# Optimization experiments

Measured on AMD Instinct MI355X. Metric: run time of the kernel, lower is better.

## Reference

```python
import jax, jax.numpy as jnp
import numpy as np

HEADS = 8
SCALE_BASE = 512
EPS = 1e-5


def xpos(x, downscale=False):
    # x: (B, h, S, hd) ; XPOS rotary embedding with exponential scale
    hd = x.shape[-1]
    S = x.shape[-2]
    half = hd // 2
    base_scale = (jnp.arange(0, hd, 2, dtype=jnp.float32) + 0.4 * hd) / (1.4 * hd)  # (half,)
    pos = jnp.arange(S, dtype=jnp.float32)
    scale = base_scale[None, :] ** (pos[:, None] / SCALE_BASE)  # (S, half)
    inv_freq = 1.0 / (10000.0 ** (jnp.arange(half, dtype=jnp.float32) / half))
    sinu = pos[:, None] * inv_freq[None, :]  # (S, half)
    sin, cos = jnp.sin(sinu), jnp.cos(sinu)
    if downscale:
        scale = 1.0 / scale
    # duplicate_interleave: (S, half) -> (S, hd)
    sin_s = jnp.repeat(sin * scale, 2, axis=-1)
    cos_s = jnp.repeat(cos * scale, 2, axis=-1)
    x1 = x[..., ::2]
    x2 = x[..., 1::2]
    rot = jnp.stack((-x2, x1), axis=-1).reshape(x.shape)  # rotate_every_two
    return x * cos_s + rot * sin_s


def decay_mask(S):
    # (heads, S, S): gamma^(n-m) for n>=m else 0
    gammas = 1.0 - jnp.exp(jnp.linspace(np.log(1 / 32), np.log(1 / 512), HEADS)).astype(jnp.float32)
    n = jnp.arange(S, dtype=jnp.float32)
    diff = n[:, None] - n[None, :]
    lg = jnp.log(gammas)[:, None, None]
    return jnp.where(diff >= 0, jnp.exp(jnp.maximum(diff, 0.0) * lg), 0.0)


def layer_norm(x, w, b):
    mu = x.mean(-1, keepdims=True)
    var = x.var(-1, keepdims=True)
    return (x - mu) / jnp.sqrt(var + EPS) * w + b


def multiscale_retention(Xq, Xkv, Wq, Wk, Wv, Wg, Wo, gn_w, gn_b):
    # Xq: (B,S,d) query source; Xkv: (B,S,d) key/value source (== Xq for self)
    B, S, _ = Xq.shape
    Q = jnp.einsum('bsd,hde->bhse', Xq, Wq)
    K = jnp.einsum('btd,hde->bhte', Xkv, Wk)
    V = jnp.einsum('btd,hdv->bhtv', Xkv, Wv)
    Q = xpos(Q)
    K = xpos(K, downscale=True)
    D = decay_mask(S)  # (h,S,S)
    scores = jnp.einsum('bhse,bhte->bhst', Q, K) * D[None]
    Y = jnp.einsum('bhst,bhtv->bhsv', scores, V)  # (B,h,S,hv)
    h, hv = Y.shape[1], Y.shape[3]
    # GroupNorm(heads, v_dim) over each head's channels per token
    mu = Y.mean(-1, keepdims=True)
    var = Y.var(-1, keepdims=True)
    Yn = (Y - mu) / jnp.sqrt(var + EPS)
    Yn = Yn.transpose(0, 2, 1, 3).reshape(B, S, h * hv) * gn_w + gn_b
    gate = jax.nn.sigmoid(Xq @ Wg) * (Xq @ Wg)  # swish gate
    return (gate * Yn) @ Wo


def setup_inputs() -> dict:
    key = jax.random.key(0)
    ks = jax.random.split(key, 32)
    d, f, h, hd, hv, vd = 1024, 4096, 8, 128, 256, 2048
    B, S = 2, 2048
    inp = {
        'X': jax.random.normal(ks[0], (B, S, d), jnp.float32),
        'mem': jax.random.normal(ks[1], (B, S, d), jnp.float32),
        'ln1_w': jax.random.uniform(ks[2], (d,), jnp.float32, 0.5, 1.5),
        'ln1_b': jax.random.normal(ks[3], (d,), jnp.float32) * 0.1,
        'ln2_w': jax.random.uniform(ks[4], (d,), jnp.float32, 0.5, 1.5),
        'ln2_b': jax.random.normal(ks[5], (d,), jnp.float32) * 0.1,
        'Wq': jax.random.normal(ks[6], (h, d, hd), jnp.float32) / d,
        'Wk': jax.random.normal(ks[7], (h, d, hd), jnp.float32) / d,
        'Wv': jax.random.normal(ks[8], (h, d, hv), jnp.float32) / d,
        'Wg': jax.random.normal(ks[9], (d, vd), jnp.float32) / d,
        'Wo': jax.random.normal(ks[10], (vd, d), jnp.float32) / d,
        'gn_w': jax.random.uniform(ks[11], (vd,), jnp.float32, 0.5, 1.5),
        'gn_b': jax.random.normal(ks[12], (vd,), jnp.float32) * 0.1,
        'cWq': jax.random.normal(ks[13], (h, d, hd), jnp.float32) / d,
        'cWk': jax.random.normal(ks[14], (h, d, hd), jnp.float32) / d,
        'cWv': jax.random.normal(ks[15], (h, d, hv), jnp.float32) / d,
        'cWg': jax.random.normal(ks[16], (d, vd), jnp.float32) / d,
        'cWo': jax.random.normal(ks[17], (vd, d), jnp.float32) / d,
        'cgn_w': jax.random.uniform(ks[18], (vd,), jnp.float32, 0.5, 1.5),
        'cgn_b': jax.random.normal(ks[19], (vd,), jnp.float32) * 0.1,
        'W1': jax.random.normal(ks[20], (d, f), jnp.float32) * (1.0 / np.sqrt(d)),
        'b1': jax.random.normal(ks[21], (f,), jnp.float32) * 0.02,
        'W2': jax.random.normal(ks[22], (f, d), jnp.float32) * (1.0 / np.sqrt(f)),
        'b2': jax.random.normal(ks[23], (d,), jnp.float32) * 0.02,
    }
    return inp


def reference(X, mem, ln1_w, ln1_b, ln2_w, ln2_b, Wq, Wk, Wv, Wg, Wo, gn_w, gn_b,
              cWq, cWk, cWv, cWg, cWo, cgn_w, cgn_b, W1, b1, W2, b2):
    # self retention block
    X = multiscale_retention(layer_norm(X, ln1_w, ln1_b), None, Wq, Wk, Wv, Wg, Wo, gn_w, gn_b) + X if False else multiscale_retention(layer_norm(X, ln1_w, ln1_b), layer_norm(X, ln1_w, ln1_b), Wq, Wk, Wv, Wg, Wo, gn_w, gn_b) + X
    # cross retention block (note: original reuses layer_norms_2 for both this and the FFN)
    h2 = layer_norm(X, ln2_w, ln2_b)
    X = multiscale_retention(h2, mem, cWq, cWk, cWv, cWg, cWo, cgn_w, cgn_b) + X
    # FFN block (GELU exact, per torch nn.GELU default)
    h3 = layer_norm(X, ln2_w, ln2_b)
    X = (jax.nn.gelu(h3 @ W1 + b1, approximate=False) @ W2 + b2) + X
    return X
```

## Files before the change

### kernel.cpp

```cpp
#include <hip/hip_runtime.h>
#include <math.h>

#define RTOT 4096
#define SEQQ 2048

typedef unsigned int uint32;
typedef __attribute__((ext_vector_type(4))) float f32x4;
typedef __attribute__((ext_vector_type(8))) short bf16x8;

__device__ __forceinline__ unsigned short f2bf(float f) {
  unsigned int u = __float_as_uint(f);
  u = (u + 0x7FFFu + ((u >> 16) & 1u)) >> 16;
  return (unsigned short)u;
}
__device__ __forceinline__ float bf2f(unsigned short h) {
  return __uint_as_float(((unsigned int)h) << 16);
}
__device__ __forceinline__ void gld16(const void* g, void* l) {
  __builtin_amdgcn_global_load_lds(
      (const __attribute__((address_space(1))) uint32*)g,
      (__attribute__((address_space(3))) uint32*)l, 16, 0, 0);
}
__device__ __forceinline__ void bar() {
  asm volatile("" ::: "memory");
  __builtin_amdgcn_s_barrier();
  asm volatile("" ::: "memory");
}
#define VMCNT(n) asm volatile("s_waitcnt vmcnt(" #n ")" ::: "memory")

__device__ __forceinline__ void tr_tile(
    const float* __restrict__ in, unsigned short* __restrict__ out,
    int R, int C, int perm, int bx, int by, int z) {
  __shared__ float t[32][33];
  in  += (size_t)z * R * C;
  out += (size_t)z * C * R;
  int r0 = bx * 32, c0 = by * 32;
  int tx = threadIdx.x & 31, ty = threadIdx.x >> 5;
  #pragma unroll
  for (int i = 0; i < 4; ++i) {
    int r = ty + i * 8;
    t[r][tx] = in[(size_t)(r0 + r) * C + c0 + tx];
  }
  __syncthreads();
  #pragma unroll
  for (int i = 0; i < 4; ++i) {
    int cc = c0 + ty + i * 8;
    if (perm) cc = 64 * (cc >> 6) + ((cc & 1) << 5) + ((cc & 63) >> 1);
    out[(size_t)cc * R + r0 + tx] = f2bf(t[tx][ty + i * 8]);
  }
}

__device__ __forceinline__ void tab_body(float* __restrict__ tab, int blk) {
  int i = blk * 256 + threadIdx.x;
  int pos = i >> 6, j = i & 63;
  float bs = (2.f * (float)j + 51.2f) * (1.f / 179.2f);
  float e = (float)pos * (1.f / 512.f);
  float sc = exp2f(e * log2f(bs));
  float invf = exp2f(-(float)j * (13.287712379549449f / 64.f));
  float su, cu;
  sincosf((float)pos * invf, &su, &cu);
  tab[i]            = cu * sc;
  tab[131072 + i]   = su * sc;
  float si = 1.f / sc;
  tab[262144 + i]   = cu * si;
  tab[393216 + i]   = su * si;
}

__global__ __launch_bounds__(256) void prep1(
    const float* Wq, const float* Wk, const float* Wg, const float* Wv,
    const float* Wo, unsigned short* WqkgT, unsigned short* WvT,
    unsigned short* WoT, float* tab) {
  int idx = blockIdx.x;
  if (idx < 1024)      { tr_tile(Wq, WqkgT,               1024, 128, 1, idx & 31, (idx >> 5) & 3, idx >> 7); }
  else if (idx < 2048) { int i = idx - 1024; tr_tile(Wk, WqkgT + 1024 * 1024, 1024, 128, 1, i & 31, (i >> 5) & 3, i >> 7); }
  else if (idx < 4096) { int i = idx - 2048; tr_tile(Wg, WqkgT + 2048 * 1024, 1024, 2048, 0, i & 31, i >> 5, 0); }
  else if (idx < 6144) { int i = idx - 4096; tr_tile(Wv, WvT, 1024, 256, 0, i & 31, (i >> 5) & 7, i >> 8); }
  else if (idx < 8192) { int i = idx - 6144; tr_tile(Wo, WoT, 2048, 1024, 0, i & 63, i >> 6, 0); }
  else                 { tab_body(tab, idx - 8192); }
}

__global__ __launch_bounds__(256) void prep2(
    const float* cWq, const float* cWg, const float* cWk, const float* cWv,
    const float* cWo, unsigned short* cQGT, unsigned short* cWkT,
    unsigned short* cWvT, unsigned short* cWoT) {
  int idx = blockIdx.x;
  if (idx < 1024)      { tr_tile(cWq, cQGT,               1024, 128, 1, idx & 31, (idx >> 5) & 3, idx >> 7); }
  else if (idx < 3072) { int i = idx - 1024; tr_tile(cWg, cQGT + 1024 * 1024, 1024, 2048, 0, i & 31, i >> 5, 0); }
  else if (idx < 4096) { int i = idx - 3072; tr_tile(cWk, cWkT, 1024, 128, 1, i & 31, (i >> 5) & 3, i >> 7); }
  else if (idx < 6144) { int i = idx - 4096; tr_tile(cWv, cWvT, 1024, 256, 0, i & 31, (i >> 5) & 7, i >> 8); }
  else                 { int i = idx - 6144; tr_tile(cWo, cWoT, 2048, 1024, 0, i & 63, i >> 6, 0); }
}

__global__ __launch_bounds__(256) void prep3(
    const float* W1, const float* W2, unsigned short* W1T, unsigned short* W2T) {
  int idx = blockIdx.x;
  if (idx < 4096) { tr_tile(W1, W1T, 1024, 4096, 0, idx & 31, idx >> 5, 0); }
  else            { int i = idx - 4096; tr_tile(W2, W2T, 4096, 1024, 0, i & 127, i >> 7, 0); }
}

__global__ __launch_bounds__(256) void cvt_bf16(
    const float* __restrict__ in, unsigned short* __restrict__ out, int n8) {
  int i = blockIdx.x * 256 + threadIdx.x;
  if (i >= n8) return;
  const float4* p = (const float4*)(in + (size_t)i * 8);
  float4 a = p[0], b = p[1];
  bf16x8 v;
  v[0] = (short)f2bf(a.x); v[1] = (short)f2bf(a.y); v[2] = (short)f2bf(a.z); v[3] = (short)f2bf(a.w);
  v[4] = (short)f2bf(b.x); v[5] = (short)f2bf(b.y); v[6] = (short)f2bf(b.z); v[7] = (short)f2bf(b.w);
  *(bf16x8*)(out + (size_t)i * 8) = v;
}

__global__ __launch_bounds__(256) void ln_bf16(const float* __restrict__ x,
    const float* __restrict__ w, const float* __restrict__ b,
    unsigned short* __restrict__ out) {
  int row = blockIdx.x, tid = threadIdx.x;
  const float* xr = x + (size_t)row * 1024;
  float4 v = *(const float4*)(xr + tid * 4);
  float s  = v.x + v.y + v.z + v.w;
  float ss = v.x*v.x + v.y*v.y + v.z*v.z + v.w*v.w;
  #pragma unroll
  for (int o = 32; o > 0; o >>= 1) { s += __shfl_down(s, o); ss += __shfl_down(ss, o); }
  __shared__ float red[2][4];
  int wid = tid >> 6;
  if ((tid & 63) == 0) { red[0][wid] = s; red[1][wid] = ss; }
  __syncthreads();
  float st  = red[0][0] + red[0][1] + red[0][2] + red[0][3];
  float sst = red[1][0] + red[1][1] + red[1][2] + red[1][3];
  float mu   = st * (1.f / 1024.f);
  float var  = sst * (1.f / 1024.f) - mu * mu;
  float rstd = rsqrtf(var + 1e-5f);
  float4 wv = *(const float4*)(w + tid * 4);
  float4 bv = *(const float4*)(b + tid * 4);
  unsigned short o0 = f2bf((v.x - mu) * rstd * wv.x + bv.x);
  unsigned short o1 = f2bf((v.y - mu) * rstd * wv.y + bv.y);
  unsigned short o2 = f2bf((v.z - mu) * rstd * wv.z + bv.z);
  unsigned short o3 = f2bf((v.w - mu) * rstd * wv.w + bv.w);
  ushort4 o4 = make_ushort4(o0, o1, o2, o3);
  *(ushort4*)(out + (size_t)row * 1024 + tid * 4) = o4;
}

enum { EPI_F32_RES = 0, EPI_BF16 = 1, EPI_XPOS = 2, EPI_GELU = 4, EPI_BRES = 5,
       EPI_QKG = 6, EPI_QG = 7 };

struct EpiP {
  void* C; int ldc;
  const float* bias; const float* resid;
  const float* tab;
  unsigned short* oQ; unsigned short* oK; unsigned short* oG;
};

template<int EPI>
__device__ __forceinline__ void epi_store(size_t m, int n, int N0, float v, const EpiP& P) {
  if constexpr (EPI == EPI_BF16) {
    ((unsigned short*)P.C)[m * P.ldc + n] = f2bf(v);
  } else if constexpr (EPI == EPI_GELU) {
    v += P.bias[n];
    v = 0.5f * v * (1.f + erff(v * 0.70710678f));
    ((unsigned short*)P.C)[m * P.ldc + n] = f2bf(v);
  } else if constexpr (EPI == EPI_BRES) {
    v += P.bias[n] + P.resid[m * P.ldc + n];
    ((float*)P.C)[m * P.ldc + n] = v;
  } else {
    v += P.resid[m * P.ldc + n];
    ((float*)P.C)[m * P.ldc + n] = v;
  }
}

template<int EPI>
__global__ __launch_bounds__(256) void gemm_mfma(
    const unsigned short* __restrict__ A, int lda,
    const unsigned short* __restrict__ Bt, int ldb, int K, int nbx, EpiP P) {
  __shared__ __align__(16) unsigned short As[2][2][128 * 32];
  __shared__ __align__(16) unsigned short Bs[2][2][128 * 32];
  const int tid = threadIdx.x, w = tid >> 6, lane = tid & 63;
  int q8 = (int)gridDim.x >> 3;
  int sbid = ((int)blockIdx.x & 7) * q8 + ((int)blockIdx.x >> 3);
  int by = sbid / nbx, bx = sbid - by * nbx;
  const int M0 = by * 128, N0 = bx * 128;
  const int fr = lane & 15, fs = lane >> 4;
  const int srow = lane >> 2, sp = lane & 3;

  f32x4 zf = {0.f, 0.f, 0.f, 0.f};
  f32x4 acc[4][4];
  #pragma unroll
  for (int i = 0; i < 4; ++i)
    #pragma unroll
    for (int j = 0; j < 4; ++j) acc[i][j] = zf;

  auto STAGE = [&](int buf, int k0) {
    #pragma unroll
    for (int kk = 0; kk < 2; ++kk)
      #pragma unroll
      for (int c = 0; c < 4; ++c) {
        int ch = w * 4 + c;
        int cc = ch & 7;
        int row = cc * 16 + srow;
        int so = sp ^ ((row >> 1) & 3);
        if (ch < 8) gld16(A  + (size_t)(M0 + row) * lda + k0 + kk * 32 + so * 8, &As[buf][kk][cc * 512]);
        else        gld16(Bt + (size_t)(N0 + row) * ldb + k0 + kk * 32 + so * 8, &Bs[buf][kk][cc * 512]);
      }
  };

  const int NT = K >> 6;
  STAGE(0, 0);
  int cur = 0;
  for (int t = 0; t < NT; ++t) {
    if (t + 1 < NT) { STAGE(cur ^ 1, (t + 1) * 64); VMCNT(8); }
    else            { VMCNT(0); }
    bar();
    #pragma unroll
    for (int kk = 0; kk < 2; ++kk) {
      bf16x8 af[4], bfr[4];
      #pragma unroll
      for (int mi = 0; mi < 4; ++mi) {
        int row = (w >> 1) * 64 + mi * 16 + fr;
        af[mi] = *(const bf16x8*)(&As[cur][kk][row * 32 + (fs ^ ((row >> 1) & 3)) * 8]);
      }
      #pragma unroll
      for (int ni = 0; ni < 4; ++ni) {
        int row = (w & 1) * 64 + ni * 16 + fr;
        bfr[ni] = *(const bf16x8*)(&Bs[cur][kk][row * 32 + (fs ^ ((row >> 1) & 3)) * 8]);
      }
      #pragma unroll
      for (int mi = 0; mi < 4; ++mi)
        #pragma unroll
        for (int ni = 0; ni < 4; ++ni)
          acc[mi][ni] = __builtin_amdgcn_mfma_f32_16x16x32_bf16(af[mi], bfr[ni], acc[mi][ni], 0, 0, 0);
    }
    bar();
    cur ^= 1;
  }

  #pragma unroll
  for (int mi = 0; mi < 4; ++mi)
    #pragma unroll
    for (int r = 0; r < 4; ++r) {
      size_t m = M0 + (w >> 1) * 64 + mi * 16 + fs * 4 + r;
      #pragma unroll
      for (int ni = 0; ni < 4; ++ni) {
        int n = N0 + (w & 1) * 64 + ni * 16 + fr;
        epi_store<EPI>(m, n, N0, acc[mi][ni][r], P);
      }
    }
}

template<int EPI>
__global__ __launch_bounds__(256) void gemm_bn64(
    const unsigned short* __restrict__ A, int lda,
    const unsigned short* __restrict__ Bt, int ldb, int K, int nbx, EpiP P) {
  __shared__ __align__(16) unsigned short As[2][2][128 * 32];
  __shared__ __align__(16) unsigned short Bs[2][2][64 * 32];
  const int tid = threadIdx.x, w = tid >> 6, lane = tid & 63;
  int q8 = (int)gridDim.x >> 3;
  int sbid = ((int)blockIdx.x & 7) * q8 + ((int)blockIdx.x >> 3);
  int by = sbid / nbx, bx = sbid - by * nbx;
  const int M0 = by * 128, N0 = bx * 64;
  const int fr = lane & 15, fs = lane >> 4;
  const int srow = lane >> 2, sp = lane & 3;

  f32x4 zf = {0.f, 0.f, 0.f, 0.f};
  f32x4 acc[2][4];
  #pragma unroll
  for (int i = 0; i < 2; ++i)
    #pragma unroll
    for (int j = 0; j < 4; ++j) acc[i][j] = zf;

  auto STAGE = [&](int buf, int k0) {
    #pragma unroll
    for (int kk = 0; kk < 2; ++kk)
      #pragma unroll
      for (int c = 0; c < 3; ++c) {
        int ch = w * 3 + c;
        if (ch < 8) {
          int row = ch * 16 + srow;
          int so = sp ^ ((row >> 1) & 3);
          gld16(A + (size_t)(M0 + row) * lda + k0 + kk * 32 + so * 8, &As[buf][kk][ch * 512]);
        } else {
          int bch = ch - 8;
          int row = bch * 16 + srow;
          int so = sp ^ ((row >> 1) & 3);
          gld16(Bt + (size_t)(N0 + row) * ldb + k0 + kk * 32 + so * 8, &Bs[buf][kk][bch * 512]);
        }
      }
  };

  const int NT = K >> 6;
  STAGE(0, 0);
  int cur = 0;
  for (int t = 0; t < NT; ++t) {
    if (t + 1 < NT) { STAGE(cur ^ 1, (t + 1) * 64); VMCNT(6); }
    else            { VMCNT(0); }
    bar();
    #pragma unroll
    for (int kk = 0; kk < 2; ++kk) {
      bf16x8 af[2], bfr[4];
      #pragma unroll
      for (int mi = 0; mi < 2; ++mi) {
        int row = w * 32 + mi * 16 + fr;
        af[mi] = *(const bf16x8*)(&As[cur][kk][row * 32 + (fs ^ ((row >> 1) & 3)) * 8]);
      }
      #pragma unroll
      for (int ni = 0; ni < 4; ++ni) {
        int row = ni * 16 + fr;
        bfr[ni] = *(const bf16x8*)(&Bs[cur][kk][row * 32 + (fs ^ ((row >> 1) & 3)) * 8]);
      }
      #pragma unroll
      for (int mi = 0; mi < 2; ++mi)
        #pragma unroll
        for (int ni = 0; ni < 4; ++ni)
          acc[mi][ni] = __builtin_amdgcn_mfma_f32_16x16x32_bf16(af[mi], bfr[ni], acc[mi][ni], 0, 0, 0);
    }
    bar();
    cur ^= 1;
  }

  if constexpr (EPI == EPI_XPOS) {
    int gsel = (N0 >> 6) & 1;
    #pragma unroll
    for (int mi = 0; mi < 2; ++mi)
      #pragma unroll
      for (int r = 0; r < 4; ++r) {
        size_t m = M0 + w * 32 + mi * 16 + fs * 4 + r;
        int pos = (int)(m & (SEQQ - 1));
        #pragma unroll
        for (int ni = 0; ni < 2; ++ni) {
          int j = gsel * 32 + ni * 16 + fr;
          float cs = P.tab[pos * 64 + j], sn = P.tab[131072 + pos * 64 + j];
          float ve = acc[mi][ni][r], vo = acc[mi][ni + 2][r];
          unsigned short* dst = (unsigned short*)P.C;
          dst[m * P.ldc + N0 + ni * 16 + fr]       = f2bf(ve * cs - vo * sn);
          dst[m * P.ldc + N0 + (ni + 2) * 16 + fr] = f2bf(vo * cs + ve * sn);
        }
      }
  } else {
    #pragma unroll
    for (int mi = 0; mi < 2; ++mi)
      #pragma unroll
      for (int r = 0; r < 4; ++r) {
        size_t m = M0 + w * 32 + mi * 16 + fs * 4 + r;
        #pragma unroll
        for (int ni = 0; ni < 4; ++ni) {
          int n = N0 + ni * 16 + fr;
          epi_store<EPI>(m, n, N0, acc[mi][ni][r], P);
        }
      }
  }
}

template<int EPI>
__global__ __launch_bounds__(512, 2) void gemm256(
    const unsigned short* __restrict__ A,
    const unsigned short* __restrict__ Bt,
    int nbx, EpiP P) {
  __shared__ __align__(16) unsigned short lds[4][2][8192];
  const int tid = threadIdx.x, w = tid >> 6, lane = tid & 63;
  int cpx = (int)gridDim.x >> 3;
  int sbid = ((int)blockIdx.x & 7) * cpx + ((int)blockIdx.x >> 3);
  int by = sbid / nbx, bx = sbid - by * nbx;
  const int M0 = by * 256, N0 = bx * 256;
  const int wm = w >> 2, wn = w & 3;
  const int fr = lane & 15, fs = lane >> 4;
  const int srow = lane >> 2;
  const int sslot = (lane & 3) ^ ((lane >> 3) & 3);
  const int rsw = (fr >> 1) & 3;

  f32x4 acc[8][4];
  #pragma unroll
  for (int i = 0; i < 8; ++i)
    #pragma unroll
    for (int j = 0; j < 4; ++j) acc[i][j] = {0.f, 0.f, 0.f, 0.f};

  auto STAGE = [&](int t, int buf) {
    int k0 = t * 32;
    #pragma unroll
    for (int j = 0; j < 4; ++j) {
      int c = w * 4 + j;
      if (c < 16)
        gld16(A  + (size_t)(M0 + c * 16 + srow) * 1024 + k0 + sslot * 8,
              &lds[buf][0][c * 512]);
      else
        gld16(Bt + (size_t)(N0 + (c - 16) * 16 + srow) * 1024 + k0 + sslot * 8,
              &lds[buf][1][(c - 16) * 512]);
    }
  };
  auto COMPUTE = [&](int t) {
    const unsigned short* la = &lds[t & 3][0][wm * 128 * 32];
    const unsigned short* lb = &lds[t & 3][1][wn * 64 * 32];
    bf16x8 a[8], b[4];
    #pragma unroll
    for (int ni = 0; ni < 4; ++ni)
      b[ni] = *(const bf16x8*)(lb + (ni * 16 + fr) * 32 + ((fs ^ rsw) * 8));
    #pragma unroll
    for (int mi = 0; mi < 8; ++mi)
      a[mi] = *(const bf16x8*)(la + (mi * 16 + fr) * 32 + ((fs ^ rsw) * 8));
    #pragma unroll
    for (int mi = 0; mi < 8; ++mi)
      #pragma unroll
      for (int ni = 0; ni < 4; ++ni)
        acc[mi][ni] = __builtin_amdgcn_mfma_f32_16x16x32_bf16(a[mi], b[ni], acc[mi][ni], 0, 0, 0);
  };

  STAGE(0, 0); STAGE(1, 1); STAGE(2, 2);
  for (int t = 0; t < 29; ++t) {
    STAGE(t + 3, (t + 3) & 3);
    VMCNT(12);
    bar();
    COMPUTE(t);
    bar();
  }
  VMCNT(8);  bar(); COMPUTE(29); bar();
  VMCNT(4);  bar(); COMPUTE(30); bar();
  VMCNT(0);  bar(); COMPUTE(31);

  if constexpr (EPI == EPI_GELU) {
    #pragma unroll
    for (int mi = 0; mi < 8; ++mi)
      #pragma unroll
      for (int r = 0; r < 4; ++r) {
        size_t m = M0 + wm * 128 + mi * 16 + fs * 4 + r;
        #pragma unroll
        for (int ni = 0; ni < 4; ++ni) {
          int n = N0 + wn * 64 + ni * 16 + fr;
          float v = acc[mi][ni][r] + P.bias[n];
          v = 0.5f * v * (1.f + erff(v * 0.70710678f));
          ((unsigned short*)P.C)[m * P.ldc + n] = f2bf(v);
        }
      }
  } else {
    const int nb = N0 + wn * 64;
    const bool isQ = nb < 1024;
    const bool isK = (EPI == EPI_QKG) && !isQ && (nb < 2048);
    if (isQ || isK) {
      const float* tc = isK ? P.tab + 262144 : P.tab;
      const float* ts = tc + 131072;
      unsigned short* dst = isK ? P.oK : P.oQ;
      const int nloc = isK ? nb - 1024 : nb;
      const int gsel = (nloc >> 6) & 1;
      #pragma unroll
      for (int mi = 0; mi < 8; ++mi)
        #pragma unroll
        for (int r = 0; r < 4; ++r) {
          size_t m = M0 + wm * 128 + mi * 16 + fs * 4 + r;
          int pos = (int)(m & (SEQQ - 1));
          #pragma unroll
          for (int ni = 0; ni < 2; ++ni) {
            int j = gsel * 32 + ni * 16 + fr;
            float cs = tc[pos * 64 + j], sn = ts[pos * 64 + j];
            float ve = acc[mi][ni][r], vo = acc[mi][ni + 2][r];
            dst[m * 1024 + nloc + ni * 16 + fr]       = f2bf(ve * cs - vo * sn);
            dst[m * 1024 + nloc + (ni + 2) * 16 + fr] = f2bf(vo * cs + ve * sn);
          }
        }
    } else {
      const int nloc = nb - ((EPI == EPI_QKG) ? 2048 : 1024);
      #pragma unroll
      for (int mi = 0; mi < 8; ++mi)
        #pragma unroll
        for (int r = 0; r < 4; ++r) {
          size_t m = M0 + wm * 128 + mi * 16 + fs * 4 + r;
          #pragma unroll
          for (int ni = 0; ni < 4; ++ni) {
            float v = acc[mi][ni][r];
            P.oG[m * 2048 + nloc + ni * 16 + fr] = f2bf(v / (1.f + expf(-v)));
          }
        }
    }
  }
}

__global__ __launch_bounds__(256) void retention_part(
    const unsigned short* __restrict__ Qx, const unsigned short* __restrict__ Kx,
    const unsigned short* __restrict__ VT,
    unsigned short* __restrict__ Y0, unsigned short* __restrict__ Y1) {
  __shared__ __align__(16) unsigned short Ks[2][32 * 128];
  __shared__ __align__(16) unsigned short Vs[2][256 * 32];
  const int tid = threadIdx.x, w = tid >> 6, lane = tid & 63;
  int bid = blockIdx.x;
  int th = bid >> 9;
  int rr = bid & 511;
  int qt, h, b;
  if (rr < 256) { qt = 31 - (rr >> 3); h = rr & 7; b = 0; }
  else          { int k = rr - 256; qt = k >> 3; h = k & 7; b = 1; }
  const int q0 = qt * 64;
  const int fr = lane & 15, fs = lane >> 4;

  float gamma = 1.f - expf(-3.4657359028f - 0.3960841032f * (float)h);
  float l2g = log2f(gamma);
  const int qglob = q0 + w * 16 + fr;

  size_t qrow = (size_t)b * SEQQ + qglob;
  bf16x8 qf[4];
  #pragma unroll
  for (int ks = 0; ks < 4; ++ks)
    qf[ks] = *(const bf16x8*)(Qx + qrow * 1024 + h * 128 + ks * 32 + fs * 8);

  float gtl8[8];
  #pragma unroll
  for (int i = 0; i < 8; ++i) {
    int toff = (i >> 2) * 16 + fs * 4 + (i & 3);
    gtl8[i] = exp2f(-(float)toff * l2g);
  }

  f32x4 zf = {0.f, 0.f, 0.f, 0.f};
  f32x4 yacc[16];
  #pragma unroll
  for (int i = 0; i < 16; ++i) yacc[i] = zf;

  int cutoff = (int)(16.f / (-l2g));
  int t_start = q0 - cutoff;
  if (t_start < 0) t_start = 0;
  t_start &= ~31;
  size_t kbase = (size_t)b * SEQQ;

  auto STAGE = [&](int buf, int t0) {
    #pragma unroll
    for (int c = 0; c < 2; ++c) {
      int ch = w * 2 + c;
      int row = ch * 4 + (lane >> 4);
      int so = (lane & 15) ^ (row & 15);
      gld16(Kx + (kbase + t0 + row) * 1024 + h * 128 + so * 8, &Ks[buf][ch * 512]);
    }
    #pragma unroll
    for (int c = 0; c < 4; ++c) {
      int ch = w * 4 + c;
      int vrow = ch * 16 + (lane >> 2);
      int so = (lane & 3) ^ ((vrow >> 1) & 3);
      gld16(VT + (size_t)(h * 256 + vrow) * RTOT + kbase + t0 + so * 8, &Vs[buf][ch * 512]);
    }
  };

  const int nt_total = (q0 + 64 - t_start) >> 5;
  const int n0 = (nt_total + 1) >> 1;
  const int it0 = th ? n0 : 0;
  const int it1 = th ? nt_total : n0;
  unsigned short* Yp = th ? Y1 : Y0;

  STAGE(0, t_start + it0 * 32);
  int cur = 0;
  for (int it = it0; it < it1; ++it) {
    int t0 = t_start + it * 32;
    if (it + 1 < it1) { STAGE(cur ^ 1, t0 + 32); VMCNT(6); }
    else              { VMCNT(0); }
    bar();

    f32x4 sacc[2];
    sacc[0] = zf; sacc[1] = zf;
    #pragma unroll
    for (int nt = 0; nt < 2; ++nt) {
      int row = nt * 16 + fr;
      #pragma unroll
      for (int ks = 0; ks < 4; ++ks) {
        int sl = ks * 4 + fs;
        bf16x8 kf = *(const bf16x8*)(&Ks[cur][row * 128 + (sl ^ (row & 15)) * 8]);
        sacc[nt] = __builtin_amdgcn_mfma_f32_16x16x32_bf16(kf, qf[ks], sacc[nt], 0, 0, 0);
      }
    }
    float fsc = exp2f((float)(qglob - t0) * l2g);
    uint32 pk[4];
    #pragma unroll
    for (int nt = 0; nt < 2; ++nt)
      #pragma unroll
      for (int hf = 0; hf < 2; ++hf) {
        int r0i = hf * 2;
        int ta = t0 + nt * 16 + fs * 4 + r0i;
        float va = (qglob >= ta)     ? sacc[nt][r0i]     * (fsc * gtl8[nt * 4 + r0i])     : 0.f;
        float vb = (qglob >= ta + 1) ? sacc[nt][r0i + 1] * (fsc * gtl8[nt * 4 + r0i + 1]) : 0.f;
        pk[nt * 2 + hf] = (uint32)f2bf(va) | ((uint32)f2bf(vb) << 16);
      }
    union { uint32 u[4]; bf16x8 v8; } pa;
    #pragma unroll
    for (int j = 0; j < 4; ++j) {
      int src = fr + 16 * (2 * (fs & 1) + (j >> 1));
      int v0 = __shfl((int)pk[j & 1],     src);
      int v1 = __shfl((int)pk[2 + (j & 1)], src);
      pa.u[j] = (fs < 2) ? (uint32)v0 : (uint32)v1;
    }
    #pragma unroll
    for (int nv = 0; nv < 16; ++nv) {
      int vrow = nv * 16 + fr;
      bf16x8 vf = *(const bf16x8*)(&Vs[cur][vrow * 32 + (fs ^ ((vrow >> 1) & 3)) * 8]);
      yacc[nv] = __builtin_amdgcn_mfma_f32_16x16x32_bf16(pa.v8, vf, yacc[nv], 0, 0, 0);
    }
    bar();
    cur ^= 1;
  }

  #pragma unroll
  for (int r = 0; r < 4; ++r) {
    int srow = q0 + w * 16 + fs * 4 + r;
    size_t mrow = (size_t)b * SEQQ + srow;
    unsigned short* orow = Yp + mrow * 2048 + h * 256;
    #pragma unroll
    for (int nv = 0; nv < 16; ++nv)
      orow[nv * 16 + fr] = f2bf(yacc[nv][r]);
  }
}

__global__ __launch_bounds__(256) void combine_gn(
    const unsigned short* __restrict__ Y0, const unsigned short* __restrict__ Y1,
    const unsigned short* __restrict__ Gate,
    const float* __restrict__ gnw, const float* __restrict__ gnb,
    unsigned short* __restrict__ Gout) {
  int idx = blockIdx.x * 4 + (threadIdx.x >> 6);
  int lane = threadIdx.x & 63;
  int h = idx & 7;
  size_t row = (size_t)(idx >> 3);
  size_t base = row * 2048 + h * 256 + lane * 4;
  ushort4 a = *(const ushort4*)(Y0 + base);
  ushort4 bb = *(const ushort4*)(Y1 + base);
  float y0 = bf2f(a.x) + bf2f(bb.x);
  float y1 = bf2f(a.y) + bf2f(bb.y);
  float y2 = bf2f(a.z) + bf2f(bb.z);
  float y3 = bf2f(a.w) + bf2f(bb.w);
  float s  = y0 + y1 + y2 + y3;
  float sq = y0*y0 + y1*y1 + y2*y2 + y3*y3;
  #pragma unroll
  for (int o = 32; o > 0; o >>= 1) { s += __shfl_xor(s, o); sq += __shfl_xor(sq, o); }
  float mu = s * (1.f / 256.f);
  float var = sq * (1.f / 256.f) - mu * mu;
  float rstd = rsqrtf(var + 1e-5f);
  int gi = h * 256 + lane * 4;
  float4 w4 = *(const float4*)(gnw + gi);
  float4 b4 = *(const float4*)(gnb + gi);
  ushort4 g4 = *(const ushort4*)(Gate + base);
  ushort4 o4;
  o4.x = f2bf(bf2f(g4.x) * ((y0 - mu) * rstd * w4.x + b4.x));
  o4.y = f2bf(bf2f(g4.y) * ((y1 - mu) * rstd * w4.y + b4.y));
  o4.z = f2bf(bf2f(g4.z) * ((y2 - mu) * rstd * w4.z + b4.z));
  o4.w = f2bf(bf2f(g4.w) * ((y3 - mu) * rstd * w4.w + b4.w));
  *(ushort4*)(Gout + base) = o4;
}

extern "C" void kernel_launch(void* const* d_in, const int* in_sizes, int n_in,
                              void* d_out, int out_size, void* d_ws, size_t ws_size,
                              hipStream_t stream) {
  const float* X    = (const float*)d_in[0];
  const float* mem  = (const float*)d_in[1];
  const float* ln1w = (const float*)d_in[2];
  const float* ln1b = (const float*)d_in[3];
  const float* ln2w = (const float*)d_in[4];
  const float* ln2b = (const float*)d_in[5];
  const float* Wq   = (const float*)d_in[6];
  const float* Wk   = (const float*)d_in[7];
  const float* Wv   = (const float*)d_in[8];
  const float* Wg   = (const float*)d_in[9];
  const float* Wo   = (const float*)d_in[10];
  const float* gnw  = (const float*)d_in[11];
  const float* gnb  = (const float*)d_in[12];
  const float* cWq  = (const float*)d_in[13];
  const float* cWk  = (const float*)d_in[14];
  const float* cWv  = (const float*)d_in[15];
  const float* cWg  = (const float*)d_in[16];
  const float* cWo  = (const float*)d_in[17];
  const float* cgnw = (const float*)d_in[18];
  const float* cgnb = (const float*)d_in[19];
  const float* W1   = (const float*)d_in[20];
  const float* b1   = (const float*)d_in[21];
  const float* W2   = (const float*)d_in[22];
  const float* b2   = (const float*)d_in[23];
  float* out = (float*)d_out;

  const size_t MB = 1024ull * 1024ull;
  if (ws_size < 106 * MB) return;
  unsigned char* W8 = (unsigned char*)d_ws;
  unsigned short* WqkgT = (unsigned short*)(W8 + 0 * MB);
  unsigned short* WvT   = (unsigned short*)(W8 + 8 * MB);
  unsigned short* WoT   = (unsigned short*)(W8 + 12 * MB);
  unsigned short* cQGT  = (unsigned short*)(W8 + 16 * MB);
  unsigned short* cWkT  = (unsigned short*)(W8 + 22 * MB);
  unsigned short* cWvT  = (unsigned short*)(W8 + 24 * MB);
  unsigned short* cWoT  = (unsigned short*)(W8 + 28 * MB);
  float*          tab   = (float*)(W8 + 32 * MB);
  unsigned short* hbuf  = (unsigned short*)(W8 + 34 * MB);
  unsigned short* Qx    = (unsigned short*)(W8 + 42 * MB);
  unsigned short* Kx    = (unsigned short*)(W8 + 50 * MB);
  unsigned short* W1T   = Qx;
  unsigned short* W2T   = Kx;
  unsigned short* VTb   = (unsigned short*)(W8 + 58 * MB);
  unsigned short* Gg    = (unsigned short*)(W8 + 74 * MB);
  unsigned short* Tb    = VTb;
  unsigned short* GoutB = (unsigned short*)(W8 + 90 * MB);
  unsigned short* mem16 = GoutB;
  unsigned short* Yp1a  = (unsigned short*)(W8 + 16 * MB);
  unsigned short* Yp1b  = (unsigned short*)(W8 + 0 * MB);

  EpiP P{};

  prep1<<<8704, 256, 0, stream>>>(Wq, Wk, Wg, Wv, Wo, WqkgT, WvT, WoT, tab);

  ln_bf16<<<RTOT, 256, 0, stream>>>(X, ln1w, ln1b, hbuf);
  P = EpiP{nullptr, 0, nullptr, nullptr, tab, Qx, Kx, Gg};
  gemm256<EPI_QKG><<<256, 512, 0, stream>>>(hbuf, WqkgT, 16, P);
  P = EpiP{VTb, 4096, nullptr, nullptr, nullptr, nullptr, nullptr, nullptr};
  gemm_mfma<EPI_BF16><<<512, 256, 0, stream>>>(WvT, 1024, hbuf, 1024, 1024, 32, P);
  retention_part<<<dim3(1024), 256, 0, stream>>>(Qx, Kx, VTb, GoutB, Yp1a);
  combine_gn<<<RTOT * 2, 256, 0, stream>>>(GoutB, Yp1a, Gg, gnw, gnb, GoutB);
  P = EpiP{out, 1024, nullptr, X, nullptr, nullptr, nullptr, nullptr};
  gemm_bn64<EPI_F32_RES><<<512, 256, 0, stream>>>(GoutB, 2048, WoT, 2048, 2048, 16, P);

  prep2<<<8192, 256, 0, stream>>>(cWq, cWg, cWk, cWv, cWo, cQGT, cWkT, cWvT, cWoT);

  cvt_bf16<<<2048, 256, 0, stream>>>(mem, mem16, 524288);
  ln_bf16<<<RTOT, 256, 0, stream>>>(out, ln2w, ln2b, hbuf);
  P = EpiP{nullptr, 0, nullptr, nullptr, tab, Qx, nullptr, Gg};
  gemm256<EPI_QG><<<192, 512, 0, stream>>>(hbuf, cQGT, 12, P);
  P = EpiP{Kx, 1024, nullptr, nullptr, tab + 262144, nullptr, nullptr, nullptr};
  gemm_bn64<EPI_XPOS><<<512, 256, 0, stream>>>(mem16, 1024, cWkT, 1024, 1024, 16, P);
  P = EpiP{VTb, 4096, nullptr, nullptr, nullptr, nullptr, nullptr, nullptr};
  gemm_mfma<EPI_BF16><<<512, 256, 0, stream>>>(cWvT, 1024, mem16, 1024, 1024, 32, P);
  retention_part<<<dim3(1024), 256, 0, stream>>>(Qx, Kx, VTb, GoutB, Yp1b);
  combine_gn<<<RTOT * 2, 256, 0, stream>>>(GoutB, Yp1b, Gg, cgnw, cgnb, GoutB);
  P = EpiP{out, 1024, nullptr, out, nullptr, nullptr, nullptr, nullptr};
  gemm_bn64<EPI_F32_RES><<<512, 256, 0, stream>>>(GoutB, 2048, cWoT, 2048, 2048, 16, P);

  prep3<<<8192, 256, 0, stream>>>(W1, W2, W1T, W2T);

  ln_bf16<<<RTOT, 256, 0, stream>>>(out, ln2w, ln2b, hbuf);
  P = EpiP{Tb, 4096, b1, nullptr, nullptr, nullptr, nullptr, nullptr};
  gemm256<EPI_GELU><<<256, 512, 0, stream>>>(hbuf, W1T, 16, P);
  P = EpiP{out, 1024, b2, out, nullptr, nullptr, nullptr, nullptr};
  gemm_bn64<EPI_BRES><<<512, 256, 0, stream>>>(Tb, 4096, W2T, 4096, 4096, 16, P);
}
```

Before: 537.2 us.

## Fuse layernorm and convert into prep kernels; retention blocks process 128 queries

Layernorm rows and the mem bf16 conversion now run as extra blocks inside the weight-transpose prep kernels, which removes several separate launches. The retention kernel now gives each block two 64-row query tiles (128 queries), so every K/V tile loaded into LDS is reused for twice as many queries, and the grid is halved. In exchange the retention kernel needs about twice as many accumulator registers, which can lower occupancy, and fewer blocks means less parallelism across the device.

```diff
diff --git a/kernel.cpp b/kernel.cpp
--- a/kernel.cpp
+++ b/kernel.cpp
@@ -66,61 +66,17 @@
   tab[393216 + i]   = su * si;
 }
 
-__global__ __launch_bounds__(256) void prep1(
-    const float* Wq, const float* Wk, const float* Wg, const float* Wv,
-    const float* Wo, unsigned short* WqkgT, unsigned short* WvT,
-    unsigned short* WoT, float* tab) {
-  int idx = blockIdx.x;
-  if (idx < 1024)      { tr_tile(Wq, WqkgT,               1024, 128, 1, idx & 31, (idx >> 5) & 3, idx >> 7); }
-  else if (idx < 2048) { int i = idx - 1024; tr_tile(Wk, WqkgT + 1024 * 1024, 1024, 128, 1, i & 31, (i >> 5) & 3, i >> 7); }
-  else if (idx < 4096) { int i = idx - 2048; tr_tile(Wg, WqkgT + 2048 * 1024, 1024, 2048, 0, i & 31, i >> 5, 0); }
-  else if (idx < 6144) { int i = idx - 4096; tr_tile(Wv, WvT, 1024, 256, 0, i & 31, (i >> 5) & 7, i >> 8); }
-  else if (idx < 8192) { int i = idx - 6144; tr_tile(Wo, WoT, 2048, 1024, 0, i & 63, i >> 6, 0); }
-  else                 { tab_body(tab, idx - 8192); }
-}
-
-__global__ __launch_bounds__(256) void prep2(
-    const float* cWq, const float* cWg, const float* cWk, const float* cWv,
-    const float* cWo, unsigned short* cQGT, unsigned short* cWkT,
-    unsigned short* cWvT, unsigned short* cWoT) {
-  int idx = blockIdx.x;
-  if (idx < 1024)      { tr_tile(cWq, cQGT,               1024, 128, 1, idx & 31, (idx >> 5) & 3, idx >> 7); }
-  else if (idx < 3072) { int i = idx - 1024; tr_tile(cWg, cQGT + 1024 * 1024, 1024, 2048, 0, i & 31, i >> 5, 0); }
-  else if (idx < 4096) { int i = idx - 3072; tr_tile(cWk, cWkT, 1024, 128, 1, i & 31, (i >> 5) & 3, i >> 7); }
-  else if (idx < 6144) { int i = idx - 4096; tr_tile(cWv, cWvT, 1024, 256, 0, i & 31, (i >> 5) & 7, i >> 8); }
-  else                 { int i = idx - 6144; tr_tile(cWo, cWoT, 2048, 1024, 0, i & 63, i >> 6, 0); }
-}
-
-__global__ __launch_bounds__(256) void prep3(
-    const float* W1, const float* W2, unsigned short* W1T, unsigned short* W2T) {
-  int idx = blockIdx.x;
-  if (idx < 4096) { tr_tile(W1, W1T, 1024, 4096, 0, idx & 31, idx >> 5, 0); }
-  else            { int i = idx - 4096; tr_tile(W2, W2T, 4096, 1024, 0, i & 127, i >> 7, 0); }
-}
-
-__global__ __launch_bounds__(256) void cvt_bf16(
-    const float* __restrict__ in, unsigned short* __restrict__ out, int n8) {
-  int i = blockIdx.x * 256 + threadIdx.x;
-  if (i >= n8) return;
-  const float4* p = (const float4*)(in + (size_t)i * 8);
-  float4 a = p[0], b = p[1];
-  bf16x8 v;
-  v[0] = (short)f2bf(a.x); v[1] = (short)f2bf(a.y); v[2] = (short)f2bf(a.z); v[3] = (short)f2bf(a.w);
-  v[4] = (short)f2bf(b.x); v[5] = (short)f2bf(b.y); v[6] = (short)f2bf(b.z); v[7] = (short)f2bf(b.w);
-  *(bf16x8*)(out + (size_t)i * 8) = v;
-}
-
-__global__ __launch_bounds__(256) void ln_bf16(const float* __restrict__ x,
+__device__ __forceinline__ void ln_row(const float* __restrict__ x,
     const float* __restrict__ w, const float* __restrict__ b,
-    unsigned short* __restrict__ out) {
-  int row = blockIdx.x, tid = threadIdx.x;
+    unsigned short* __restrict__ out, int row) {
+  __shared__ float red[2][4];
+  int tid = threadIdx.x;
   const float* xr = x + (size_t)row * 1024;
   float4 v = *(const float4*)(xr + tid * 4);
   float s  = v.x + v.y + v.z + v.w;
   float ss = v.x*v.x + v.y*v.y + v.z*v.z + v.w*v.w;
   #pragma unroll
   for (int o = 32; o > 0; o >>= 1) { s += __shfl_down(s, o); ss += __shfl_down(ss, o); }
-  __shared__ float red[2][4];
   int wid = tid >> 6;
   if ((tid & 63) == 0) { red[0][wid] = s; red[1][wid] = ss; }
   __syncthreads();
@@ -139,6 +95,57 @@
   *(ushort4*)(out + (size_t)row * 1024 + tid * 4) = o4;
 }
 
+__device__ __forceinline__ void cvt_body(const float* __restrict__ in,
+    unsigned short* __restrict__ out, int blk) {
+  int i = blk * 256 + threadIdx.x;
+  const float4* p = (const float4*)(in + (size_t)i * 8);
+  float4 a = p[0], b = p[1];
+  bf16x8 v;
+  v[0] = (short)f2bf(a.x); v[1] = (short)f2bf(a.y); v[2] = (short)f2bf(a.z); v[3] = (short)f2bf(a.w);
+  v[4] = (short)f2bf(b.x); v[5] = (short)f2bf(b.y); v[6] = (short)f2bf(b.z); v[7] = (short)f2bf(b.w);
+  *(bf16x8*)(out + (size_t)i * 8) = v;
+}
+
+__global__ __launch_bounds__(256) void prep1(
+    const float* Wq, const float* Wk, const float* Wg, const float* Wv,
+    const float* Wo, unsigned short* WqkgT, unsigned short* WvT,
+    unsigned short* WoT, float* tab,
+    const float* X, const float* ln1w, const float* ln1b, unsigned short* hbuf) {
+  int idx = blockIdx.x;
+  if (idx < 1024)      { tr_tile(Wq, WqkgT,               1024, 128, 1, idx & 31, (idx >> 5) & 3, idx >> 7); }
+  else if (idx < 2048) { int i = idx - 1024; tr_tile(Wk, WqkgT + 1024 * 1024, 1024, 128, 1, i & 31, (i >> 5) & 3, i >> 7); }
+  else if (idx < 4096) { int i = idx - 2048; tr_tile(Wg, WqkgT + 2048 * 1024, 1024, 2048, 0, i & 31, i >> 5, 0); }
+  else if (idx < 6144) { int i = idx - 4096; tr_tile(Wv, WvT, 1024, 256, 0, i & 31, (i >> 5) & 7, i >> 8); }
+  else if (idx < 8192) { int i = idx - 6144; tr_tile(Wo, WoT, 2048, 1024, 0, i & 63, i >> 6, 0); }
+  else if (idx < 8704) { tab_body(tab, idx - 8192); }
+  else                 { ln_row(X, ln1w, ln1b, hbuf, idx - 8704); }
+}
+
+__global__ __launch_bounds__(256) void prep2(
+    const float* cWq, const float* cWg, const float* cWk, const float* cWv,
+    const float* cWo, unsigned short* cQGT, unsigned short* cWkT,
+    unsigned short* cWvT, unsigned short* cWoT,
+    const float* mem, unsigned short* mem16,
+    const float* out, const float* ln2w, const float* ln2b, unsigned short* hbuf) {
+  int idx = blockIdx.x;
+  if (idx < 1024)       { tr_tile(cWq, cQGT,               1024, 128, 1, idx & 31, (idx >> 5) & 3, idx >> 7); }
+  else if (idx < 3072)  { int i = idx - 1024; tr_tile(cWg, cQGT + 1024 * 1024, 1024, 2048, 0, i & 31, i >> 5, 0); }
+  else if (idx < 4096)  { int i = idx - 3072; tr_tile(cWk, cWkT, 1024, 128, 1, i & 31, (i >> 5) & 3, i >> 7); }
+  else if (idx < 6144)  { int i = idx - 4096; tr_tile(cWv, cWvT, 1024, 256, 0, i & 31, (i >> 5) & 7, i >> 8); }
+  else if (idx < 8192)  { int i = idx - 6144; tr_tile(cWo, cWoT, 2048, 1024, 0, i & 63, i >> 6, 0); }
+  else if (idx < 10240) { cvt_body(mem, mem16, idx - 8192); }
+  else                  { ln_row(out, ln2w, ln2b, hbuf, idx - 10240); }
+}
+
+__global__ __launch_bounds__(256) void prep3(
+    const float* W1, const float* W2, unsigned short* W1T, unsigned short* W2T,
+    const float* out, const float* ln2w, const float* ln2b, unsigned short* hbuf) {
+  int idx = blockIdx.x;
+  if (idx < 4096)      { tr_tile(W1, W1T, 1024, 4096, 0, idx & 31, idx >> 5, 0); }
+  else if (idx < 8192) { int i = idx - 4096; tr_tile(W2, W2T, 4096, 1024, 0, i & 127, i >> 7, 0); }
+  else                 { ln_row(out, ln2w, ln2b, hbuf, idx - 8192); }
+}
+
 enum { EPI_F32_RES = 0, EPI_BF16 = 1, EPI_XPOS = 2, EPI_GELU = 4, EPI_BRES = 5,
        EPI_QKG = 6, EPI_QG = 7 };
 
@@ -476,23 +483,27 @@
   __shared__ __align__(16) unsigned short Vs[2][256 * 32];
   const int tid = threadIdx.x, w = tid >> 6, lane = tid & 63;
   int bid = blockIdx.x;
-  int th = bid >> 9;
-  int rr = bid & 511;
-  int qt, h, b;
-  if (rr < 256) { qt = 31 - (rr >> 3); h = rr & 7; b = 0; }
-  else          { int k = rr - 256; qt = k >> 3; h = k & 7; b = 1; }
-  const int q0 = qt * 64;
+  int th = bid >> 8;
+  int rr = bid & 255;
+  int b  = rr >> 7;
+  int rl = rr & 127;
+  int qt = th ? (rl >> 3) : (15 - (rl >> 3));
+  int h  = rl & 7;
+  const int q0 = qt * 128;
   const int fr = lane & 15, fs = lane >> 4;
 
   float gamma = 1.f - expf(-3.4657359028f - 0.3960841032f * (float)h);
   float l2g = log2f(gamma);
-  const int qglob = q0 + w * 16 + fr;
-
-  size_t qrow = (size_t)b * SEQQ + qglob;
-  bf16x8 qf[4];
-  #pragma unroll
-  for (int ks = 0; ks < 4; ++ks)
-    qf[ks] = *(const bf16x8*)(Qx + qrow * 1024 + h * 128 + ks * 32 + fs * 8);
+  const int qA = q0 + w * 16 + fr;
+  const int qB = qA + 64;
+
+  size_t rowA = (size_t)b * SEQQ + qA;
+  bf16x8 qfA[4], qfB[4];
+  #pragma unroll
+  for (int ks = 0; ks < 4; ++ks) {
+    qfA[ks] = *(const bf16x8*)(Qx + rowA * 1024 + h * 128 + ks * 32 + fs * 8);
+    qfB[ks] = *(const bf16x8*)(Qx + (rowA + 64) * 1024 + h * 128 + ks * 32 + fs * 8);
+  }
 
   float gtl8[8];
   #pragma unroll
@@ -502,9 +513,9 @@
   }
 
   f32x4 zf = {0.f, 0.f, 0.f, 0.f};
-  f32x4 yacc[16];
-  #pragma unroll
-  for (int i = 0; i < 16; ++i) yacc[i] = zf;
+  f32x4 yA[16], yB[16];
+  #pragma unroll
+  for (int i = 0; i < 16; ++i) { yA[i] = zf; yB[i] = zf; }
 
   int cutoff = (int)(16.f / (-l2g));
   int t_start = q0 - cutoff;
@@ -529,7 +540,7 @@
     }
   };
 
-  const int nt_total = (q0 + 64 - t_start) >> 5;
+  const int nt_total = (q0 + 128 - t_start) >> 5;
   const int n0 = (nt_total + 1) >> 1;
   const int it0 = th ? n0 : 0;
   const int it1 = th ? nt_total : n0;
@@ -543,8 +554,8 @@
     else              { VMCNT(0); }
     bar();
 
-    f32x4 sacc[2];
-    sacc[0] = zf; sacc[1] = zf;
+    f32x4 sA[2], sB[2];
+    sA[0] = zf; sA[1] = zf; sB[0] = zf; sB[1] = zf;
     #pragma unroll
     for (int nt = 0; nt < 2; ++nt) {
       int row = nt * 16 + fr;
@@ -552,34 +563,45 @@
       for (int ks = 0; ks < 4; ++ks) {
         int sl = ks * 4 + fs;
         bf16x8 kf = *(const bf16x8*)(&Ks[cur][row * 128 + (sl ^ (row & 15)) * 8]);
-        sacc[nt] = __builtin_amdgcn_mfma_f32_16x16x32_bf16(kf, qf[ks], sacc[nt], 0, 0, 0);
-      }
-    }
-    float fsc = exp2f((float)(qglob - t0) * l2g);
-    uint32 pk[4];
+        sA[nt] = __builtin_amdgcn_mfma_f32_16x16x32_bf16(kf, qfA[ks], sA[nt], 0, 0, 0);
+        sB[nt] = __builtin_amdgcn_mfma_f32_16x16x32_bf16(kf, qfB[ks], sB[nt], 0, 0, 0);
+      }
+    }
+    float fscA = exp2f((float)(qA - t0) * l2g);
+    float fscB = exp2f((float)(qB - t0) * l2g);
+    uint32 pkA[4], pkB[4];
     #pragma unroll
     for (int nt = 0; nt < 2; ++nt)
       #pragma unroll
       for (int hf = 0; hf < 2; ++hf) {
         int r0i = hf * 2;
         int ta = t0 + nt * 16 + fs * 4 + r0i;
-        float va = (qglob >= ta)     ? sacc[nt][r0i]     * (fsc * gtl8[nt * 4 + r0i])     : 0.f;
-        float vb = (qglob >= ta + 1) ? sacc[nt][r0i + 1] * (fsc * gtl8[nt * 4 + r0i + 1]) : 0.f;
-        pk[nt * 2 + hf] = (uint32)f2bf(va) | ((uint32)f2bf(vb) << 16);
-      }
-    union { uint32 u[4]; bf16x8 v8; } pa;
+        float g0 = fscA * gtl8[nt * 4 + r0i], g1 = fscA * gtl8[nt * 4 + r0i + 1];
+        float va = (qA >= ta)     ? sA[nt][r0i]     * g0 : 0.f;
+        float vb = (qA >= ta + 1) ? sA[nt][r0i + 1] * g1 : 0.f;
+        pkA[nt * 2 + hf] = (uint32)f2bf(va) | ((uint32)f2bf(vb) << 16);
+        float h0 = fscB * gtl8[nt * 4 + r0i], h1 = fscB * gtl8[nt * 4 + r0i + 1];
+        float vc = (qB >= ta)     ? sB[nt][r0i]     * h0 : 0.f;
+        float vd = (qB >= ta + 1) ? sB[nt][r0i + 1] * h1 : 0.f;
+        pkB[nt * 2 + hf] = (uint32)f2bf(vc) | ((uint32)f2bf(vd) << 16);
+      }
+    union { uint32 u[4]; bf16x8 v8; } paA, paB;
     #pragma unroll
     for (int j = 0; j < 4; ++j) {
       int src = fr + 16 * (2 * (fs & 1) + (j >> 1));
-      int v0 = __shfl((int)pk[j & 1],     src);
-      int v1 = __shfl((int)pk[2 + (j & 1)], src);
-      pa.u[j] = (fs < 2) ? (uint32)v0 : (uint32)v1;
+      int a0 = __shfl((int)pkA[j & 1],       src);
+      int a1 = __shfl((int)pkA[2 + (j & 1)], src);
+      paA.u[j] = (fs < 2) ? (uint32)a0 : (uint32)a1;
+      int b0 = __shfl((int)pkB[j & 1],       src);
+      int b1 = __shfl((int)pkB[2 + (j & 1)], src);
+      paB.u[j] = (fs < 2) ? (uint32)b0 : (uint32)b1;
     }
     #pragma unroll
     for (int nv = 0; nv < 16; ++nv) {
       int vrow = nv * 16 + fr;
       bf16x8 vf = *(const bf16x8*)(&Vs[cur][vrow * 32 + (fs ^ ((vrow >> 1) & 3)) * 8]);
-      yacc[nv] = __builtin_amdgcn_mfma_f32_16x16x32_bf16(pa.v8, vf, yacc[nv], 0, 0, 0);
+      yA[nv] = __builtin_amdgcn_mfma_f32_16x16x32_bf16(paA.v8, vf, yA[nv], 0, 0, 0);
+      yB[nv] = __builtin_amdgcn_mfma_f32_16x16x32_bf16(paB.v8, vf, yB[nv], 0, 0, 0);
     }
     bar();
     cur ^= 1;
@@ -587,12 +609,15 @@
 
   #pragma unroll
   for (int r = 0; r < 4; ++r) {
-    int srow = q0 + w * 16 + fs * 4 + r;
-    size_t mrow = (size_t)b * SEQQ + srow;
-    unsigned short* orow = Yp + mrow * 2048 + h * 256;
-    #pragma unroll
-    for (int nv = 0; nv < 16; ++nv)
-      orow[nv * 16 + fr] = f2bf(yacc[nv][r]);
+    int sra = q0 + w * 16 + fs * 4 + r;
+    size_t mra = (size_t)b * SEQQ + sra;
+    unsigned short* oa = Yp + mra * 2048 + h * 256;
+    unsigned short* ob = Yp + (mra + 64) * 2048 + h * 256;
+    #pragma unroll
+    for (int nv = 0; nv < 16; ++nv) {
+      oa[nv * 16 + fr] = f2bf(yA[nv][r]);
+      ob[nv * 16 + fr] = f2bf(yB[nv][r]);
+    }
   }
 }
 
@@ -686,36 +711,34 @@
 
   EpiP P{};
 
-  prep1<<<8704, 256, 0, stream>>>(Wq, Wk, Wg, Wv, Wo, WqkgT, WvT, WoT, tab);
-
-  ln_bf16<<<RTOT, 256, 0, stream>>>(X, ln1w, ln1b, hbuf);
+  prep1<<<12800, 256, 0, stream>>>(Wq, Wk, Wg, Wv, Wo, WqkgT, WvT, WoT, tab,
+                                   X, ln1w, ln1b, hbuf);
+
   P = EpiP{nullptr, 0, nullptr, nullptr, tab, Qx, Kx, Gg};
   gemm256<EPI_QKG><<<256, 512, 0, stream>>>(hbuf, WqkgT, 16, P);
   P = EpiP{VTb, 4096, nullptr, nullptr, nullptr, nullptr, nullptr, nullptr};
   gemm_mfma<EPI_BF16><<<512, 256, 0, stream>>>(WvT, 1024, hbuf, 1024, 1024, 32, P);
-  retention_part<<<dim3(1024), 256, 0, stream>>>(Qx, Kx, VTb, GoutB, Yp1a);
+  retention_part<<<dim3(512), 256, 0, stream>>>(Qx, Kx, VTb, GoutB, Yp1a);
   combine_gn<<<RTOT * 2, 256, 0, stream>>>(GoutB, Yp1a, Gg, gnw, gnb, GoutB);
   P = EpiP{out, 1024, nullptr, X, nullptr, nullptr, nullptr, nullptr};
   gemm_bn64<EPI_F32_RES><<<512, 256, 0, stream>>>(GoutB, 2048, WoT, 2048, 2048, 16, P);
 
-  prep2<<<8192, 256, 0, stream>>>(cWq, cWg, cWk, cWv, cWo, cQGT, cWkT, cWvT, cWoT);
-
-  cvt_bf16<<<2048, 256, 0, stream>>>(mem, mem16, 524288);
-  ln_bf16<<<RTOT, 256, 0, stream>>>(out, ln2w, ln2b, hbuf);
+  prep2<<<14336, 256, 0, stream>>>(cWq, cWg, cWk, cWv, cWo, cQGT, cWkT, cWvT, cWoT,
+                                   mem, mem16, out, ln2w, ln2b, hbuf);
+
   P = EpiP{nullptr, 0, nullptr, nullptr, tab, Qx, nullptr, Gg};
   gemm256<EPI_QG><<<192, 512, 0, stream>>>(hbuf, cQGT, 12, P);
   P = EpiP{Kx, 1024, nullptr, nullptr, tab + 262144, nullptr, nullptr, nullptr};
   gemm_bn64<EPI_XPOS><<<512, 256, 0, stream>>>(mem16, 1024, cWkT, 1024, 1024, 16, P);
   P = EpiP{VTb, 4096, nullptr, nullptr, nullptr, nullptr, nullptr, nullptr};
   gemm_mfma<EPI_BF16><<<512, 256, 0, stream>>>(cWvT, 1024, mem16, 1024, 1024, 32, P);
-  retention_part<<<dim3(1024), 256, 0, stream>>>(Qx, Kx, VTb, GoutB, Yp1b);
+  retention_part<<<dim3(512), 256, 0, stream>>>(Qx, Kx, VTb, GoutB, Yp1b);
   combine_gn<<<RTOT * 2, 256, 0, stream>>>(GoutB, Yp1b, Gg, cgnw, cgnb, GoutB);
   P = EpiP{out, 1024, nullptr, out, nullptr, nullptr, nullptr, nullptr};
   gemm_bn64<EPI_F32_RES><<<512, 256, 0, stream>>>(GoutB, 2048, cWoT, 2048, 2048, 16, P);
 
-  prep3<<<8192, 256, 0, stream>>>(W1, W2, W1T, W2T);
-
-  ln_bf16<<<RTOT, 256, 0, stream>>>(out, ln2w, ln2b, hbuf);
+  prep3<<<12288, 256, 0, stream>>>(W1, W2, W1T, W2T, out, ln2w, ln2b, hbuf);
+
   P = EpiP{Tb, 4096, b1, nullptr, nullptr, nullptr, nullptr, nullptr};
   gemm256<EPI_GELU><<<256, 512, 0, stream>>>(hbuf, W1T, 16, P);
   P = EpiP{out, 1024, b2, out, nullptr, nullptr, nullptr, nullptr};
```

Result: slower. 588.5 us (+9.6%).
